# Kernel tuning notes

Hardware: AMD Instinct MI355X
Metric: run time of the kernel (lower is better)

## Reference

```python
import jax, jax.numpy as jnp
import numpy as np


def setup_inputs() -> dict:
    key = jax.random.key(0)
    k1, k2 = jax.random.split(key)
    batch, cw_dim = 4096, 1024
    dim_embedding, book_size = 8, 256
    dim_codes = cw_dim // dim_embedding  # 128
    x = jax.random.normal(k1, (batch, cw_dim), dtype=jnp.float32)
    codebook = jax.random.normal(k2, (dim_codes, book_size, dim_embedding), dtype=jnp.float32)
    return {"x": x, "codebook": codebook}


def reference(x, codebook):
    # Faithful JAX version of VQVAE.quantise:
    #   pairwise squared distance -> argmin -> gather embeddings -> one-hot scatter
    C, K, D = codebook.shape          # dim_codes, book_size, dim_embedding
    B = x.shape[0]
    xr = x.reshape(B, C, D)           # [B, C, D] (= view(batch*dim_codes, 1, D))
    x2 = jnp.sum(xr * xr, axis=-1)                       # [B, C]
    c2 = jnp.sum(codebook * codebook, axis=-1)           # [C, K]
    dist = x2[..., None] - 2.0 * jnp.einsum('bcd,ckd->bck', xr, codebook) + c2[None]
    idx = jnp.argmin(dist, axis=-1)                      # [B, C]
    # gather nearest codebook entry per code slot
    cw_embed = codebook[jnp.arange(C)[None, :], idx]     # [B, C, D]
    cw_embed = cw_embed.reshape(B, C * D)                # [B, cw_dim]
    # one-hot scatter of selected indices
    one_hot_idx = jax.nn.one_hot(idx, K, dtype=jnp.float32)  # [B, C, K]
    return cw_embed, one_hot_idx
```

## Files before the change

### kernel.cpp

```cpp
#include <hip/hip_runtime.h>


constexpr int B_    = 4096;
constexpr int C_    = 128;
constexpr int K_    = 256;
constexpr int D_    = 8;
constexpr int TPB   = 256;
constexpr int BPT   = 4;
constexpr int BTILE = TPB * BPT;

__global__ __launch_bounds__(TPB, 2) void vq_kernel(
    const float* __restrict__ x,
    const float* __restrict__ cb,
    float* __restrict__ out_embed,
    float* __restrict__ out_onehot)
{
    __shared__ float  s_cbf[K_ * D_];
    __shared__ double s_cbd[K_ * D_];
    __shared__ double s_c2d[K_];

    const int c     = blockIdx.x;
    const int btile = blockIdx.y;
    const int tid   = threadIdx.x;

    {
        const float4* gcb = (const float4*)(cb + (size_t)c * (K_ * D_));
        const float4 v0 = gcb[tid];
        const float4 v1 = gcb[tid + TPB];
        ((float4*)s_cbf)[tid]       = v0;
        ((float4*)s_cbf)[tid + TPB] = v1;
        const int i0 = tid * 4, i1 = (tid + TPB) * 4;
        s_cbd[i0 + 0] = (double)v0.x;
        s_cbd[i0 + 1] = (double)v0.y;
        s_cbd[i0 + 2] = (double)v0.z;
        s_cbd[i0 + 3] = (double)v0.w;
        s_cbd[i1 + 0] = (double)v1.x;
        s_cbd[i1 + 1] = (double)v1.y;
        s_cbd[i1 + 2] = (double)v1.z;
        s_cbd[i1 + 3] = (double)v1.w;
    }
    __syncthreads();

    {
        const double* v = s_cbd + tid * D_;
        double s = 0.0;
        #pragma unroll
        for (int d = 0; d < D_; ++d) s = fma(v[d], v[d], s);
        s_c2d[tid] = s;
    }
    __syncthreads();

    double xd[BPT][D_];
    #pragma unroll
    for (int j = 0; j < BPT; ++j) {
        const int b = btile * BTILE + j * TPB + tid;
        const float4* xp = (const float4*)(x + (size_t)b * (C_ * D_) + c * D_);
        const float4 a = xp[0];
        const float4 h = xp[1];
        xd[j][0] = (double)a.x; xd[j][1] = (double)a.y;
        xd[j][2] = (double)a.z; xd[j][3] = (double)a.w;
        xd[j][4] = (double)h.x; xd[j][5] = (double)h.y;
        xd[j][6] = (double)h.z; xd[j][7] = (double)h.w;
    }

    double best[BPT];
    int    bidx[BPT];
    #pragma unroll
    for (int j = 0; j < BPT; ++j) { best[j] = 1.0e300; bidx[j] = 0; }

    for (int k = 0; k < K_; ++k) {
        double cd[D_];
        #pragma unroll
        for (int d = 0; d < D_; ++d) cd[d] = s_cbd[k * D_ + d];
        const double c2k = s_c2d[k];
        #pragma unroll
        for (int j = 0; j < BPT; ++j) {
            double dot = xd[j][0] * cd[0];
            #pragma unroll
            for (int d = 1; d < D_; ++d) dot = fma(xd[j][d], cd[d], dot);
            const double score = fma(-2.0, dot, c2k);
            if (score < best[j]) { best[j] = score; bidx[j] = k; }
        }
    }

    const float4* scbf4 = (const float4*)s_cbf;
    #pragma unroll
    for (int j = 0; j < BPT; ++j) {
        const int    b    = btile * BTILE + j * TPB + tid;
        const size_t pair = (size_t)b * C_ + c;
        const int    kmin = bidx[j];

        float4* dst = (float4*)(out_embed + pair * D_);
        dst[0] = scbf4[kmin * 2];
        dst[1] = scbf4[kmin * 2 + 1];

        float4* oh = (float4*)(out_onehot + pair * K_);
        const int ch = kmin >> 2;
        const int r  = kmin & 3;
        float4 one4;
        one4.x = (r == 0) ? 1.f : 0.f;
        one4.y = (r == 1) ? 1.f : 0.f;
        one4.z = (r == 2) ? 1.f : 0.f;
        one4.w = (r == 3) ? 1.f : 0.f;
        const float4 zero4 = make_float4(0.f, 0.f, 0.f, 0.f);
        #pragma unroll 8
        for (int t = 0; t < K_ / 4; ++t) {
            oh[t] = (t == ch) ? one4 : zero4;
        }
    }
}

extern "C" void kernel_launch(void* const* d_in, const int* in_sizes, int n_in,
                              void* d_out, int out_size, void* d_ws, size_t ws_size,
                              hipStream_t stream) {
    const float* x  = (const float*)d_in[0];
    const float* cb = (const float*)d_in[1];
    float* out        = (float*)d_out;
    float* out_embed  = out;
    float* out_onehot = out + (size_t)B_ * C_ * D_;

    dim3 grid(C_, B_ / BTILE);
    vq_kernel<<<grid, TPB, 0, stream>>>(x, cb, out_embed, out_onehot);
}
```

Before: 710.9 us.

## Split argmin and output writes into two kernels with coalesced one-hot stores

```diff
diff --git a/kernel.cpp b/kernel.cpp
--- a/kernel.cpp
+++ b/kernel.cpp
@@ -9,13 +9,11 @@
 constexpr int BPT   = 4;
 constexpr int BTILE = TPB * BPT;
 
-__global__ __launch_bounds__(TPB, 2) void vq_kernel(
+__global__ __launch_bounds__(TPB, 2) void vq_argmin(
     const float* __restrict__ x,
     const float* __restrict__ cb,
-    float* __restrict__ out_embed,
-    float* __restrict__ out_onehot)
+    int* __restrict__ idx_out)
 {
-    __shared__ float  s_cbf[K_ * D_];
     __shared__ double s_cbd[K_ * D_];
     __shared__ double s_c2d[K_];
 
@@ -27,17 +25,11 @@
         const float4* gcb = (const float4*)(cb + (size_t)c * (K_ * D_));
         const float4 v0 = gcb[tid];
         const float4 v1 = gcb[tid + TPB];
-        ((float4*)s_cbf)[tid]       = v0;
-        ((float4*)s_cbf)[tid + TPB] = v1;
         const int i0 = tid * 4, i1 = (tid + TPB) * 4;
-        s_cbd[i0 + 0] = (double)v0.x;
-        s_cbd[i0 + 1] = (double)v0.y;
-        s_cbd[i0 + 2] = (double)v0.z;
-        s_cbd[i0 + 3] = (double)v0.w;
-        s_cbd[i1 + 0] = (double)v1.x;
-        s_cbd[i1 + 1] = (double)v1.y;
-        s_cbd[i1 + 2] = (double)v1.z;
-        s_cbd[i1 + 3] = (double)v1.w;
+        s_cbd[i0 + 0] = (double)v0.x; s_cbd[i0 + 1] = (double)v0.y;
+        s_cbd[i0 + 2] = (double)v0.z; s_cbd[i0 + 3] = (double)v0.w;
+        s_cbd[i1 + 0] = (double)v1.x; s_cbd[i1 + 1] = (double)v1.y;
+        s_cbd[i1 + 2] = (double)v1.z; s_cbd[i1 + 3] = (double)v1.w;
     }
     __syncthreads();
 
@@ -79,34 +71,58 @@
             #pragma unroll
             for (int d = 1; d < D_; ++d) dot = fma(xd[j][d], cd[d], dot);
             const double score = fma(-2.0, dot, c2k);
-            if (score < best[j]) { best[j] = score; bidx[j] = k; }
+            const bool lt = score < best[j];
+            best[j] = lt ? score : best[j];
+            bidx[j] = lt ? k : bidx[j];
         }
     }
 
-    const float4* scbf4 = (const float4*)s_cbf;
     #pragma unroll
     for (int j = 0; j < BPT; ++j) {
-        const int    b    = btile * BTILE + j * TPB + tid;
-        const size_t pair = (size_t)b * C_ + c;
-        const int    kmin = bidx[j];
+        const int b = btile * BTILE + j * TPB + tid;
+        idx_out[(size_t)b * C_ + c] = bidx[j];
+    }
+}
 
-        float4* dst = (float4*)(out_embed + pair * D_);
-        dst[0] = scbf4[kmin * 2];
-        dst[1] = scbf4[kmin * 2 + 1];
+constexpr int GRID2 = 2048;
+constexpr int RPB   = (B_ * C_) / GRID2;
 
-        float4* oh = (float4*)(out_onehot + pair * K_);
-        const int ch = kmin >> 2;
-        const int r  = kmin & 3;
-        float4 one4;
-        one4.x = (r == 0) ? 1.f : 0.f;
-        one4.y = (r == 1) ? 1.f : 0.f;
-        one4.z = (r == 2) ? 1.f : 0.f;
-        one4.w = (r == 3) ? 1.f : 0.f;
-        const float4 zero4 = make_float4(0.f, 0.f, 0.f, 0.f);
-        #pragma unroll 8
-        for (int t = 0; t < K_ / 4; ++t) {
-            oh[t] = (t == ch) ? one4 : zero4;
-        }
+__global__ __launch_bounds__(TPB, 4) void vq_write(
+    const int*   __restrict__ idx,
+    const float* __restrict__ cb,
+    float* __restrict__ out_embed,
+    float* __restrict__ out_onehot)
+{
+    const int tid  = threadIdx.x;
+    const int lane = tid & 63;
+    const int wave = tid >> 6;
+    const int blk  = blockIdx.x;
+
+    const int rowbase = blk * RPB + wave * 64;
+    const int myk = idx[rowbase + lane];
+    const int e0 = lane * 4;
+    #pragma unroll 4
+    for (int i = 0; i < 64; ++i) {
+        const int k = __builtin_amdgcn_readlane(myk, i);
+        float4 v;
+        v.x = (k == e0    ) ? 1.f : 0.f;
+        v.y = (k == e0 + 1) ? 1.f : 0.f;
+        v.z = (k == e0 + 2) ? 1.f : 0.f;
+        v.w = (k == e0 + 3) ? 1.f : 0.f;
+        ((float4*)(out_onehot + (size_t)(rowbase + i) * K_))[lane] = v;
+    }
+
+    const size_t pbase = (size_t)blk * RPB;
+    #pragma unroll
+    for (int i = 0; i < 2; ++i) {
+        const int    f    = i * TPB + tid;
+        const int    pl   = f >> 1;
+        const int    half = f & 1;
+        const size_t pair = pbase + pl;
+        const int    c    = (int)(pair & (C_ - 1));
+        const int    k    = idx[pair];
+        const float4 val  = ((const float4*)(cb + ((size_t)c * K_ + k) * D_))[half];
+        ((float4*)(out_embed + pbase * D_))[f] = val;
     }
 }
 
@@ -118,7 +134,10 @@
     float* out        = (float*)d_out;
     float* out_embed  = out;
     float* out_onehot = out + (size_t)B_ * C_ * D_;
+    int*   idx_ws     = (int*)d_ws;
 
-    dim3 grid(C_, B_ / BTILE);
-    vq_kernel<<<grid, TPB, 0, stream>>>(x, cb, out_embed, out_onehot);
+    dim3 grid1(C_, B_ / BTILE);
+    vq_argmin<<<grid1, TPB, 0, stream>>>(x, cb, idx_ws);
+
+    vq_write<<<GRID2, TPB, 0, stream>>>(idx_ws, cb, out_embed, out_onehot);
 }
```

Result: faster. 617.8 us (-13.1%).
